# Kernel optimization log

Hardware: AMD Instinct MI355X
Metric: run time of the kernel (lower is better)

## Reference

```python
import jax, jax.numpy as jnp
import numpy as np

TW = 25          # time_window
H = 128          # hidden_features
NL = 6           # hidden_layer
N = 8192         # batch*n_nodes
E = 131072       # edges (avg degree 16)
EDGE_DIM = 51    # 50 (u diff) + 1 (pos_x diff)
LEM_IN = 4       # pos_x, u_ch0, u_ch1, ts
PDE_L = 16.0
PDE_TMAX = 4.0
PDE_DT = 0.04
NEG_SLOPE = 0.2  # PyG GATConv leaky_relu slope


def swish(x):
    return x * jax.nn.sigmoid(x)


def setup_inputs() -> dict:
    key = jax.random.key(0)
    ks = jax.random.split(key, 32)
    def p(k, shape, s=0.05):
        return jax.random.normal(k, shape, jnp.float32) * s
    inp = {}
    inp['u'] = jax.random.normal(ks[0], (N, 2 * TW), jnp.float32)
    inp['pos'] = jax.random.uniform(ks[1], (N, 2), jnp.float32)
    inp['edge_index'] = jax.random.randint(ks[2], (2, E), 0, N)
    # LEM cell params (inp2hid: 4H, hid2hid: 3H, transform_z: H)
    inp['lem_inp_w'] = p(ks[3], (4 * H, LEM_IN)); inp['lem_inp_b'] = jnp.zeros(4 * H, jnp.float32)
    inp['lem_hid_w'] = p(ks[4], (3 * H, H));      inp['lem_hid_b'] = jnp.zeros(3 * H, jnp.float32)
    inp['lem_z_w'] = p(ks[5], (H, H));            inp['lem_z_b'] = jnp.zeros(H, jnp.float32)
    # lemoutput_mlp
    inp['mlp1_w'] = p(ks[6], (H, H)); inp['mlp1_b'] = jnp.zeros(H, jnp.float32)
    inp['mlp2_w'] = p(ks[7], (H, H)); inp['mlp2_b'] = jnp.zeros(H, jnp.float32)
    # main GAT layers (stacked over NL)
    inp['gnn_lin_w'] = p(ks[8], (NL, H, H)); inp['gnn_edge_w'] = p(ks[9], (NL, H, EDGE_DIM))
    inp['gnn_att_src'] = p(ks[10], (NL, H)); inp['gnn_att_dst'] = p(ks[11], (NL, H))
    inp['gnn_att_edge'] = p(ks[12], (NL, H)); inp['gnn_bias'] = jnp.zeros((NL, H), jnp.float32)
    # gate GAT layers
    inp['gate_lin_w'] = p(ks[13], (NL, H, H)); inp['gate_edge_w'] = p(ks[14], (NL, H, EDGE_DIM))
    inp['gate_att_src'] = p(ks[15], (NL, H)); inp['gate_att_dst'] = p(ks[16], (NL, H))
    inp['gate_att_edge'] = p(ks[17], (NL, H)); inp['gate_bias'] = jnp.zeros((NL, H), jnp.float32)
    # double_mlp + conv1d decoder (time_window==25 branch)
    inp['dbl_w'] = p(ks[18], (2 * H, H)); inp['dbl_b'] = jnp.zeros(2 * H, jnp.float32)
    inp['conv1_w'] = p(ks[19], (8, 2, 16)); inp['conv1_b'] = jnp.zeros(8, jnp.float32)
    inp['conv2_w'] = p(ks[20], (2, 8, 14)); inp['conv2_b'] = jnp.zeros(2, jnp.float32)
    return inp


def _gat(x, src, dst, edge_attr, lin_w, edge_w, a_src, a_dst, a_edge, bias):
    """Single-head GATConv with edge features (PyG semantics, aggregate at dst)."""
    xt = x @ lin_w.T                      # [N,H]
    et = edge_attr @ edge_w.T             # [E,H]
    logits = jax.nn.leaky_relu((xt @ a_src)[src] + (xt @ a_dst)[dst] + et @ a_edge, NEG_SLOPE)
    amax = jax.ops.segment_max(logits, dst, num_segments=N)
    amax = jnp.where(jnp.isfinite(amax), amax, 0.0)
    ex = jnp.exp(logits - amax[dst])
    denom = jax.ops.segment_sum(ex, dst, num_segments=N)
    w = ex / (denom[dst] + 1e-16)         # edge softmax over incoming edges
    out = jax.ops.segment_sum(w[:, None] * xt[src], dst, num_segments=N)
    return out + bias


def _forward(u, pos, lem_inp_w, lem_inp_b, lem_hid_w, lem_hid_b, lem_z_w, lem_z_b,
             mlp1_w, mlp1_b, mlp2_w, mlp2_b,
             gnn_lin_w, gnn_edge_w, gnn_att_src, gnn_att_dst, gnn_att_edge, gnn_bias,
             gate_lin_w, gate_edge_w, gate_att_src, gate_att_dst, gate_att_edge, gate_bias,
             dbl_w, dbl_b, conv1_w, conv1_b, conv2_w, conv2_b, edge_index):
    pos_x = pos[:, 1:2] / PDE_L    # [N,1]
    pos_t = pos[:, 0:1] / PDE_TMAX # [N,1]
    dt = jnp.cumsum(jnp.full((TW,), PDE_DT, jnp.float32))  # [TW]
    ts = pos_t + dt[None, :]       # [N,TW]
    # LEM input: [TW, N, 4] = (pos_x, u channel 0, u channel 1, ts)
    lem_x = jnp.concatenate([
        jnp.broadcast_to(pos_x[None, :, :], (TW, N, 1)),
        u[:, :TW].T[:, :, None],
        u[:, TW:].T[:, :, None],
        ts.T[:, :, None],
    ], axis=-1)

    def cell(carry, xt):
        y, z = carry
        ii = xt @ lem_inp_w.T + lem_inp_b   # [N,4H]
        hh = y @ lem_hid_w.T + lem_hid_b    # [N,3H]
        i1, i2, i3, i4 = jnp.split(ii, 4, axis=-1)
        h1, h2, h3 = jnp.split(hh, 3, axis=-1)
        ms_dt_bar = jax.nn.sigmoid(i1 + h1)
        ms_dt = jax.nn.sigmoid(i2 + h2)
        z = (1.0 - ms_dt) * z + ms_dt * jnp.tanh(i3 + h3)
        y = (1.0 - ms_dt_bar) * y + ms_dt_bar * jnp.tanh(z @ lem_z_w.T + lem_z_b + i4)
        return (y, z), None

    y0 = jnp.zeros((N, H), u.dtype)
    (y, _), _ = jax.lax.scan(cell, (y0, y0), lem_x)
    h = swish(y @ mlp1_w.T + mlp1_b)
    h = swish(h @ mlp2_w.T + mlp2_b)

    src, dst = edge_index[0], edge_index[1]
    edge_attr = jnp.concatenate([u[src] - u[dst], pos_x[src] - pos_x[dst]], axis=-1)  # [E,51]

    for i in range(NL):
        tau = jax.nn.sigmoid(_gat(h, src, dst, edge_attr, gate_lin_w[i], gate_edge_w[i],
                                  gate_att_src[i], gate_att_dst[i], gate_att_edge[i], gate_bias[i]))
        msg = swish(_gat(h, src, dst, edge_attr, gnn_lin_w[i], gnn_edge_w[i],
                         gnn_att_src[i], gnn_att_dst[i], gnn_att_edge[i], gnn_bias[i]))
        h = (1.0 - tau) * h + tau * msg

    h2 = swish(h @ dbl_w.T + dbl_b).reshape(N, 2, H)  # [N,2,128]
    dn = ('NCH', 'OIH', 'NCH')
    d = jax.lax.conv_general_dilated(h2, conv1_w, (3,), 'VALID', dimension_numbers=dn)
    d = swish(d + conv1_b[None, :, None])              # [N,8,38]
    d = jax.lax.conv_general_dilated(d, conv2_w, (1,), 'VALID', dimension_numbers=dn)
    d = d + conv2_b[None, :, None]                     # [N,2,25]
    out = u.reshape(N, 2, TW) + dt[None, None, :] * d
    return out.reshape(N, 2 * TW)


def reference(u, pos, edge_index, lem_inp_w, lem_inp_b, lem_hid_w, lem_hid_b, lem_z_w, lem_z_b,
              mlp1_w, mlp1_b, mlp2_w, mlp2_b,
              gnn_lin_w, gnn_edge_w, gnn_att_src, gnn_att_dst, gnn_att_edge, gnn_bias,
              gate_lin_w, gate_edge_w, gate_att_src, gate_att_dst, gate_att_edge, gate_bias,
              dbl_w, dbl_b, conv1_w, conv1_b, conv2_w, conv2_b):
    return _forward(u, pos, lem_inp_w, lem_inp_b, lem_hid_w, lem_hid_b, lem_z_w, lem_z_b,
                    mlp1_w, mlp1_b, mlp2_w, mlp2_b,
                    gnn_lin_w, gnn_edge_w, gnn_att_src, gnn_att_dst, gnn_att_edge, gnn_bias,
                    gate_lin_w, gate_edge_w, gate_att_src, gate_att_dst, gate_att_edge, gate_bias,
                    dbl_w, dbl_b, conv1_w, conv1_b, conv2_w, conv2_b, edge_index)
```

## Files before the change

kernel.cpp:

```cpp
#include <hip/hip_runtime.h>

#define N_NODES 8192
#define N_EDGES 131072

using short8 = __attribute__((ext_vector_type(8))) short;
using f32x4  = __attribute__((ext_vector_type(4))) float;

__device__ __forceinline__ float rcpf(float x){ return __builtin_amdgcn_rcpf(x); }
__device__ __forceinline__ float sigm(float x){ return rcpf(1.0f+__expf(-x)); }
__device__ __forceinline__ float ftanh(float x){ float e=__expf(2.0f*x); return (e-1.0f)*rcpf(e+1.0f); }
__device__ __forceinline__ float swishf(float x){ return x*sigm(x); }
__device__ __forceinline__ float leaky(float x){ return x>=0.0f? x : 0.2f*x; }
__device__ __forceinline__ float dot4(float4 a, float4 b){ return a.x*b.x+a.y*b.y+a.z*b.z+a.w*b.w; }
__device__ __forceinline__ short f2bf(float x){
  unsigned u=__float_as_uint(x);
  unsigned r=(u + 0x7fffu + ((u>>16)&1u))>>16;
  return (short)r;
}
__device__ __forceinline__ int pack2bf(float a, float b){
  return (int)(((unsigned)(unsigned short)f2bf(a)) | (((unsigned)(unsigned short)f2bf(b))<<16));
}

__device__ __forceinline__ float wave_rmax(float v){
  #pragma unroll
  for(int m=32;m;m>>=1) v=fmaxf(v,__shfl_xor(v,m));
  return v;
}
__device__ __forceinline__ float wave_rsum(float v){
  #pragma unroll
  for(int m=32;m;m>>=1) v+=__shfl_xor(v,m);
  return v;
}

__global__ __launch_bounds__(256) void hist_kernel(const int* __restrict__ dst, int* __restrict__ cnt){
  int e=blockIdx.x*256+threadIdx.x;
  if(e<N_EDGES) atomicAdd(&cnt[dst[e]],1);
}

__global__ __launch_bounds__(1024) void scan_kernel(const int* __restrict__ cnt, int* __restrict__ rowptr, int* __restrict__ cursor){
  __shared__ int sums[1024];
  int t=threadIdx.x; int base=t*8;
  int local[8]; int s=0;
  #pragma unroll
  for(int i=0;i<8;++i){ local[i]=s; s+=cnt[base+i]; }
  sums[t]=s; __syncthreads();
  for(int off=1;off<1024;off<<=1){
    int v=(t>=off)?sums[t-off]:0;
    __syncthreads();
    sums[t]+=v;
    __syncthreads();
  }
  int offset=(t>0)?sums[t-1]:0;
  #pragma unroll
  for(int i=0;i<8;++i){ int v=offset+local[i]; rowptr[base+i]=v; cursor[base+i]=v; }
  if(t==1023) rowptr[N_NODES]=sums[1023];
}

__global__ __launch_bounds__(256) void scatter_kernel(const int* __restrict__ src, const int* __restrict__ dst,
                                                      int* __restrict__ cursor, int* __restrict__ csr_src){
  int e=blockIdx.x*256+threadIdx.x;
  if(e<N_EDGES){
    int slot=atomicAdd(&cursor[dst[e]],1);
    csr_src[slot]=src[e];
  }
}

__global__ __launch_bounds__(256) void prep_bf16_kernel(
    const float* __restrict__ lem_hid_w, const float* __restrict__ lem_z_w,
    const float* __restrict__ mlp1_w, const float* __restrict__ mlp2_w,
    const float* __restrict__ gate_lin_w, const float* __restrict__ gnn_lin_w,
    short* __restrict__ whb, short* __restrict__ wzb, short* __restrict__ w1b,
    short* __restrict__ w2b, short* __restrict__ wlin16)
{
  int i=blockIdx.x*256+threadIdx.x;
  if(i<49152){ whb[i]=f2bf(lem_hid_w[i]); return; }
  if(i<65536){ int k=i-49152; wzb[k]=f2bf(lem_z_w[k]); return; }
  if(i<81920){ int k=i-65536; w1b[k]=f2bf(mlp1_w[k]); return; }
  if(i<98304){ int k=i-81920; w2b[k]=f2bf(mlp2_w[k]); return; }
  int k=i-98304;
  int l=k>>15, which=(k>>14)&1, r=k&16383;
  const float* s = which? gnn_lin_w + l*16384 + r : gate_lin_w + l*16384 + r;
  wlin16[k]=f2bf(*s);
}

__global__ __launch_bounds__(256) void we_kernel(const float* __restrict__ gate_ew, const float* __restrict__ gnn_ew,
                                                 const float* __restrict__ gate_ae, const float* __restrict__ gnn_ae,
                                                 float* __restrict__ we){
  int idx=blockIdx.x*256+threadIdx.x;
  if(idx>=12*51) return;
  int g=idx/51, k=idx%51, l=g>>1;
  const float* ew = (g&1)? gnn_ew + l*128*51 : gate_ew + l*128*51;
  const float* ae = (g&1)? gnn_ae + l*128    : gate_ae + l*128;
  float s=0.f;
  for(int f=0;f<128;++f) s+=ew[f*51+k]*ae[f];
  we[idx]=s;
}

__global__ __launch_bounds__(128) void gsc_kernel(const float* __restrict__ u, const float* __restrict__ pos,
                                                  const float* __restrict__ we, float* __restrict__ gsc){
  int n=blockIdx.x*128+threadIdx.x;
  float uv[50];
  #pragma unroll
  for(int k=0;k<50;++k) uv[k]=u[n*50+k];
  float px=pos[n*2+1]*(1.0f/16.0f);
  for(int g=0;g<12;++g){
    const float* w=we+g*51;
    float s=w[50]*px;
    #pragma unroll
    for(int k=0;k<50;++k) s+=w[k]*uv[k];
    gsc[g*N_NODES+n]=s;
  }
}

__global__ __launch_bounds__(512,2) void lem_mfma2_kernel(
    const float* __restrict__ u, const float* __restrict__ pos,
    const float* __restrict__ Wi, const float* __restrict__ bi,
    const short* __restrict__ whb, const float* __restrict__ bh,
    const short* __restrict__ wzb, const float* __restrict__ bz,
    const short* __restrict__ w1b, const float* __restrict__ b1,
    const short* __restrict__ w2b, const float* __restrict__ b2,
    float* __restrict__ hout)
{
  __shared__ short y16[16*128];
  __shared__ short z16[16*128];
  __shared__ float u_s[16*50];
  __shared__ float hstg[16*132];

  const int tid=threadIdx.x, lane=tid&63, w=tid>>6;
  const int node=lane&15, q=lane>>4;
  const int n7=node&7;
  const int n0=blockIdx.x*16;

  for(int i=tid;i<16*50;i+=512) u_s[i]=u[n0*50+i];
  for(int i=tid;i<16*64;i+=512) ((int*)y16)[i]=0;

  const float px = pos[(n0+node)*2+1]*(1.0f/16.0f);
  const float pt = pos[(n0+node)*2+0]*0.25f;

  float cbase[4][4], cslope[4][4], ca[4][4], cb[4][4];
  #pragma unroll
  for(int gg=0; gg<4; ++gg){
    #pragma unroll
    for(int r=0;r<4;++r){
      int fr = w*16+q*4+r;
      int row = gg*128+fr;
      float4 wi = *(const float4*)(Wi+4*row);
      float bb = bi[row] + ((gg<3)? bh[row] : bz[fr]);
      cbase[gg][r] = bb + wi.x*px + wi.w*pt;
      cslope[gg][r]= wi.w*0.04f;
      ca[gg][r]=wi.y; cb[gg][r]=wi.z;
    }
  }

  short8 whf[3][4];
  #pragma unroll
  for(int gg=0;gg<3;++gg)
    #pragma unroll
    for(int kk=0;kk<4;++kk)
      whf[gg][kk]=*(const short8*)(whb + (gg*128 + w*16 + node)*128 + kk*32 + q*8);
  short8 wzf[4];
  #pragma unroll
  for(int kk=0;kk<4;++kk)
    wzf[kk]=*(const short8*)(wzb + (w*16 + node)*128 + kk*32 + q*8);

  float yreg[4]={0.f,0.f,0.f,0.f}, zreg[4]={0.f,0.f,0.f,0.f};
  float msb[4], i4s[4];
  const int wrslot = (w*16+q*4) ^ (n7<<3);
  __syncthreads();

  for(int t=0;t<25;++t){
    f32x4 h1a={0.f,0.f,0.f,0.f}, h2a=h1a, h3a=h1a;
    #pragma unroll
    for(int kk=0;kk<4;++kk){
      short8 yb=*(const short8*)&y16[node*128 + ((kk*32 + q*8) ^ (n7<<3))];
      h1a=__builtin_amdgcn_mfma_f32_16x16x32_bf16(whf[0][kk],yb,h1a,0,0,0);
      h2a=__builtin_amdgcn_mfma_f32_16x16x32_bf16(whf[1][kk],yb,h2a,0,0,0);
      h3a=__builtin_amdgcn_mfma_f32_16x16x32_bf16(whf[2][kk],yb,h3a,0,0,0);
    }
    const float u0=u_s[node*50+t], u1=u_s[node*50+25+t];
    const float tf=(float)(t+1);
    #pragma unroll
    for(int r=0;r<4;++r){
      float i1=cbase[0][r]+cslope[0][r]*tf+ca[0][r]*u0+cb[0][r]*u1;
      float i2=cbase[1][r]+cslope[1][r]*tf+ca[1][r]*u0+cb[1][r]*u1;
      float i3=cbase[2][r]+cslope[2][r]*tf+ca[2][r]*u0+cb[2][r]*u1;
      i4s[r]  =cbase[3][r]+cslope[3][r]*tf+ca[3][r]*u0+cb[3][r]*u1;
      msb[r]=sigm(i1+h1a[r]);
      float ms=sigm(i2+h2a[r]);
      zreg[r]=(1.0f-ms)*zreg[r]+ms*ftanh(i3+h3a[r]);
    }
    { int2 zz; zz.x=pack2bf(zreg[0],zreg[1]); zz.y=pack2bf(zreg[2],zreg[3]);
      *(int2*)&z16[node*128 + wrslot]=zz; }
    __syncthreads();
    f32x4 zw={0.f,0.f,0.f,0.f};
    #pragma unroll
    for(int kk=0;kk<4;++kk){
      short8 zb=*(const short8*)&z16[node*128 + ((kk*32 + q*8) ^ (n7<<3))];
      zw=__builtin_amdgcn_mfma_f32_16x16x32_bf16(wzf[kk],zb,zw,0,0,0);
    }
    #pragma unroll
    for(int r=0;r<4;++r)
      yreg[r]=(1.0f-msb[r])*yreg[r]+msb[r]*ftanh(zw[r]+i4s[r]);
    { int2 yy; yy.x=pack2bf(yreg[0],yreg[1]); yy.y=pack2bf(yreg[2],yreg[3]);
      *(int2*)&y16[node*128 + wrslot]=yy; }
    __syncthreads();
  }

  {
    short8 w1f[4];
    #pragma unroll
    for(int kk=0;kk<4;++kk)
      w1f[kk]=*(const short8*)(w1b + (w*16 + node)*128 + kk*32 + q*8);
    float4 b1v=*(const float4*)(b1 + w*16 + q*4);
    f32x4 a={0.f,0.f,0.f,0.f};
    #pragma unroll
    for(int kk=0;kk<4;++kk){
      short8 yb=*(const short8*)&y16[node*128 + ((kk*32 + q*8) ^ (n7<<3))];
      a=__builtin_amdgcn_mfma_f32_16x16x32_bf16(w1f[kk],yb,a,0,0,0);
    }
    float t0=swishf(a[0]+b1v.x), t1=swishf(a[1]+b1v.y);
    float t2=swishf(a[2]+b1v.z), t3=swishf(a[3]+b1v.w);
    int2 zz; zz.x=pack2bf(t0,t1); zz.y=pack2bf(t2,t3);
    *(int2*)&z16[node*128 + wrslot]=zz;
  }
  __syncthreads();
  {
    short8 w2f[4];
    #pragma unroll
    for(int kk=0;kk<4;++kk)
      w2f[kk]=*(const short8*)(w2b + (w*16 + node)*128 + kk*32 + q*8);
    float4 b2v=*(const float4*)(b2 + w*16 + q*4);
    f32x4 a={0.f,0.f,0.f,0.f};
    #pragma unroll
    for(int kk=0;kk<4;++kk){
      short8 zb=*(const short8*)&z16[node*128 + ((kk*32 + q*8) ^ (n7<<3))];
      a=__builtin_amdgcn_mfma_f32_16x16x32_bf16(w2f[kk],zb,a,0,0,0);
    }
    hstg[node*132 + w*16+q*4+0]=swishf(a[0]+b2v.x);
    hstg[node*132 + w*16+q*4+1]=swishf(a[1]+b2v.y);
    hstg[node*132 + w*16+q*4+2]=swishf(a[2]+b2v.z);
    hstg[node*132 + w*16+q*4+3]=swishf(a[3]+b2v.w);
  }
  __syncthreads();
  for(int i=tid;i<16*128;i+=512){
    int nn=i>>7, ff=i&127;
    hout[(n0+nn)*128+ff]=hstg[nn*132+ff];
  }
}

__global__ __launch_bounds__(256) void gat_transform_mfma(
    const float* __restrict__ h,
    const short* __restrict__ wl,
    const float* __restrict__ a_sg, const float* __restrict__ a_dg,
    const float* __restrict__ a_sm, const float* __restrict__ a_dm,
    const float* __restrict__ gsc_g, const float* __restrict__ gsc_m,
    short* __restrict__ xt16, float* __restrict__ ss2, float* __restrict__ sd2)
{
  __shared__ short h16[32*128];
  __shared__ short xts[32*256];
  const int tid=threadIdx.x, lane=tid&63, w=tid>>6;
  const int rt=w&1, cg=w>>1;
  const int r16=lane&15, kq=lane>>4;
  const int n0=blockIdx.x*32;

  {
    const float4* hp=(const float4*)(h + (size_t)n0*128) + tid*4;
    int row=tid>>3, e0=(tid&7)*16;
    #pragma unroll
    for(int c=0;c<2;++c){
      float4 v0=hp[2*c], v1=hp[2*c+1];
      short8 s;
      s[0]=f2bf(v0.x); s[1]=f2bf(v0.y); s[2]=f2bf(v0.z); s[3]=f2bf(v0.w);
      s[4]=f2bf(v1.x); s[5]=f2bf(v1.y); s[6]=f2bf(v1.z); s[7]=f2bf(v1.w);
      *(short8*)&h16[row*128 + ((e0+8*c) ^ ((row&7)<<3))]=s;
    }
  }
  __syncthreads();
  short8 afr[4];
  {
    int row=rt*16+r16;
    #pragma unroll
    for(int kk=0;kk<4;++kk)
      afr[kk]=*(const short8*)&h16[row*128 + ((kk*32+kq*8) ^ ((row&7)<<3))];
  }
  const short* wb = wl + cg*16384;
  const float* as_ = cg? a_sm : a_sg;
  const float* ad_ = cg? a_dm : a_dg;
  float ssp[4]={0,0,0,0}, sdp[4]={0,0,0,0};
  #pragma unroll
  for(int ct=0;ct<8;++ct){
    int c0=ct*16;
    f32x4 acc={0.f,0.f,0.f,0.f};
    #pragma unroll
    for(int kk=0;kk<4;++kk){
      short8 b=*(const short8*)(wb + (c0+r16)*128 + kk*32 + kq*8);
      acc=__builtin_amdgcn_mfma_f32_16x16x32_bf16(afr[kk],b,acc,0,0,0);
    }
    float av=as_[c0+r16], dv=ad_[c0+r16];
    #pragma unroll
    for(int r=0;r<4;++r){
      ssp[r]+=acc[r]*av; sdp[r]+=acc[r]*dv;
      xts[(rt*16+kq*4+r)*256 + cg*128 + c0 + r16]=f2bf(acc[r]);
    }
  }
  #pragma unroll
  for(int m=1;m<16;m<<=1){
    #pragma unroll
    for(int r=0;r<4;++r){
      ssp[r]+=__shfl_xor(ssp[r],m);
      sdp[r]+=__shfl_xor(sdp[r],m);
    }
  }
  if(r16==0){
    #pragma unroll
    for(int r=0;r<4;++r){
      int n=n0+rt*16+kq*4+r;
      float gv = (cg? gsc_m : gsc_g)[n];
      ss2[2*n+cg]=ssp[r]+gv;
      sd2[2*n+cg]=sdp[r]-gv;
    }
  }
  __syncthreads();
  const short8* sp=(const short8*)xts;
  short8* dp=(short8*)(xt16 + (size_t)n0*256);
  for(int i=tid;i<32*256/8;i+=256) dp[i]=sp[i];
}

__global__ __launch_bounds__(256) void gat_aggregate2(
    const int* __restrict__ rowptr, const int* __restrict__ csr_src,
    const short* __restrict__ xt16,
    const float* __restrict__ ss2, const float* __restrict__ sd2,
    const float* __restrict__ bias_g, const float* __restrict__ bias_m,
    float* __restrict__ h)
{
  __shared__ float4 stg[4][64];
  const int lane=threadIdx.x&63, w=threadIdx.x>>6;
  const int n=blockIdx.x*4+w;
  const int s0=rowptr[n], deg=rowptr[n+1]-s0;
  const float2 sdv=*(const float2*)(sd2+2*n);
  const float bg=sdv.x, bm=sdv.y;

  float mg=-1e30f, mm=-1e30f;
  int sc=0; float lgc=0.f, lmc=0.f;
  for(int c=0;c<deg;c+=64){
    int i=c+lane;
    if(i<deg){
      int s=csr_src[s0+i];
      float2 ssv=*(const float2*)(ss2+2*s);
      float lg=leaky(ssv.x+bg), lm=leaky(ssv.y+bm);
      if(c==0){sc=s; lgc=lg; lmc=lm;}
      mg=fmaxf(mg,lg); mm=fmaxf(mm,lm);
    }
  }
  mg=wave_rmax(mg); mm=wave_rmax(mm);

  float dg=0.f, dm=0.f;
  float acc0=0.f,acc1=0.f,acc2=0.f,acc3=0.f;
  for(int c=0;c<deg;c+=64){
    int i=c+lane;
    int s=sc; float lg=lgc, lm=lmc;
    if(c>0 && i<deg){
      s=csr_src[s0+i];
      float2 ssv=*(const float2*)(ss2+2*s);
      lg=leaky(ssv.x+bg); lm=leaky(ssv.y+bm);
    }
    float eg=0.f, em=0.f;
    if(i<deg){ eg=__expf(lg-mg); em=__expf(lm-mm); dg+=eg; dm+=em; }
    float4 st; st.x=__int_as_float(s); st.y=eg; st.z=em; st.w=0.f;
    stg[w][lane]=st;
    __threadfence_block();
    int cntc=min(64,deg-c);
    for(int j=0;j<cntc;++j){
      float4 e=stg[w][j];
      int sj=__float_as_int(e.x);
      float wgt = lane<32 ? e.y : e.z;
      const unsigned* xp=(const unsigned*)(xt16 + (size_t)sj*256 + 4*lane);
      unsigned p0=xp[0], p1=xp[1];
      acc0 += wgt*__uint_as_float(p0<<16);
      acc1 += wgt*__uint_as_float(p0&0xffff0000u);
      acc2 += wgt*__uint_as_float(p1<<16);
      acc3 += wgt*__uint_as_float(p1&0xffff0000u);
    }
  }
  dg=wave_rsum(dg); dm=wave_rsum(dm);
  float rr = lane<32? rcpf(dg+1e-16f) : rcpf(dm+1e-16f);
  const float* bp = lane<32 ? bias_g + 4*lane : bias_m + 4*(lane-32);
  float4 bv=*(const float4*)bp;
  float o0=acc0*rr+bv.x, o1=acc1*rr+bv.y, o2=acc2*rr+bv.z, o3=acc3*rr+bv.w;
  float s0_=sigm(o0), s1_=sigm(o1), s2_=sigm(o2), s3_=sigm(o3);
  float v0 = lane<32? s0_ : o0*s0_;
  float v1 = lane<32? s1_ : o1*s1_;
  float v2 = lane<32? s2_ : o2*s2_;
  float v3 = lane<32? s3_ : o3*s3_;
  float m0=__shfl_xor(v0,32), m1=__shfl_xor(v1,32), m2=__shfl_xor(v2,32), m3=__shfl_xor(v3,32);
  if(lane<32){
    float4 hv=*(const float4*)(h + (size_t)n*128 + 4*lane);
    hv.x=(1.0f-v0)*hv.x+v0*m0;
    hv.y=(1.0f-v1)*hv.y+v1*m1;
    hv.z=(1.0f-v2)*hv.z+v2*m2;
    hv.w=(1.0f-v3)*hv.w+v3*m3;
    *(float4*)(h + (size_t)n*128 + 4*lane)=hv;
  }
}

__global__ __launch_bounds__(256) void decoder_kernel(
    const float* __restrict__ h, const float* __restrict__ u,
    const float* __restrict__ Wd, const float* __restrict__ bd,
    const float* __restrict__ w1, const float* __restrict__ b1,
    const float* __restrict__ w2, const float* __restrict__ b2,
    float* __restrict__ out)
{
  __shared__ float h_lds[8][128];
  __shared__ float h2[8][2][128];
  __shared__ float c1[8][8][38];
  __shared__ float w1s[256], w2s[224], b1s[8], b2s[2];
  const int tid=threadIdx.x;
  const int n0=blockIdx.x*8;
  for(int i=tid;i<8*128;i+=256) ((float*)h_lds)[i]=h[n0*128+i];
  w1s[tid]=w1[tid];
  if(tid<224) w2s[tid]=w2[tid];
  if(tid<8) b1s[tid]=b1[tid];
  if(tid<2) b2s[tid]=b2[tid];
  __syncthreads();
  {
    const float4* wp=(const float4*)(Wd + tid*128);
    float acc[8];
    #pragma unroll
    for(int n=0;n<8;++n)acc[n]=0.f;
    for(int k=0;k<32;++k){
      float4 w=wp[k];
      #pragma unroll
      for(int n=0;n<8;++n){ float4 hv=*(const float4*)&h_lds[n][k*4]; acc[n]+=dot4(w,hv); }
    }
    float bdv=bd[tid];
    int ch=tid>>7, p=tid&127;
    #pragma unroll
    for(int n=0;n<8;++n) h2[n][ch][p]=swishf(acc[n]+bdv);
  }
  __syncthreads();
  for(int idx=tid; idx<8*8*38; idx+=256){
    int n=idx/(8*38); int r=idx%(8*38); int oc=r/38, p=r%38;
    float acc=b1s[oc];
    const float* ww=&w1s[oc*32];
    #pragma unroll
    for(int ic=0;ic<2;++ic)
      #pragma unroll
      for(int k=0;k<16;++k) acc+=ww[ic*16+k]*h2[n][ic][3*p+k];
    c1[n][oc][p]=swishf(acc);
  }
  __syncthreads();
  for(int idx=tid; idx<8*2*25; idx+=256){
    int n=idx/50; int r=idx%50; int oc=r/25, p=r%25;
    float acc=b2s[oc];
    const float* ww=&w2s[oc*112];
    #pragma unroll
    for(int ic=0;ic<8;++ic)
      #pragma unroll
      for(int k=0;k<14;++k) acc+=ww[ic*14+k]*c1[n][ic][p+k];
    int col=oc*25+p;
    out[(n0+n)*50+col]=u[(n0+n)*50+col]+0.04f*(float)(p+1)*acc;
  }
}

extern "C" void kernel_launch(void* const* d_in, const int* in_sizes, int n_in,
                              void* d_out, int out_size, void* d_ws, size_t ws_size,
                              hipStream_t stream)
{
  const float* u          =(const float*)d_in[0];
  const float* pos        =(const float*)d_in[1];
  const int*   ei         =(const int*)d_in[2];
  const float* lem_inp_w  =(const float*)d_in[3];
  const float* lem_inp_b  =(const float*)d_in[4];
  const float* lem_hid_w  =(const float*)d_in[5];
  const float* lem_hid_b  =(const float*)d_in[6];
  const float* lem_z_w    =(const float*)d_in[7];
  const float* lem_z_b    =(const float*)d_in[8];
  const float* mlp1_w     =(const float*)d_in[9];
  const float* mlp1_b     =(const float*)d_in[10];
  const float* mlp2_w     =(const float*)d_in[11];
  const float* mlp2_b     =(const float*)d_in[12];
  const float* gnn_lin_w  =(const float*)d_in[13];
  const float* gnn_edge_w =(const float*)d_in[14];
  const float* gnn_att_src=(const float*)d_in[15];
  const float* gnn_att_dst=(const float*)d_in[16];
  const float* gnn_att_edge=(const float*)d_in[17];
  const float* gnn_bias   =(const float*)d_in[18];
  const float* gate_lin_w =(const float*)d_in[19];
  const float* gate_edge_w=(const float*)d_in[20];
  const float* gate_att_src=(const float*)d_in[21];
  const float* gate_att_dst=(const float*)d_in[22];
  const float* gate_att_edge=(const float*)d_in[23];
  const float* gate_bias  =(const float*)d_in[24];
  const float* dbl_w      =(const float*)d_in[25];
  const float* dbl_b      =(const float*)d_in[26];
  const float* conv1_w    =(const float*)d_in[27];
  const float* conv1_b    =(const float*)d_in[28];
  const float* conv2_w    =(const float*)d_in[29];
  const float* conv2_b    =(const float*)d_in[30];
  float* out=(float*)d_out;

  char* ws=(char*)d_ws;
  size_t off=0;
  auto alloc=[&](size_t bytes)->char*{ char* p=ws+off; off+=(bytes+255)&~(size_t)255; return p; };
  float* h    =(float*)alloc((size_t)N_NODES*128*4);
  short* xt16 =(short*)alloc((size_t)N_NODES*256*2);
  float* ss2  =(float*)alloc((size_t)N_NODES*2*4);
  float* sd2  =(float*)alloc((size_t)N_NODES*2*4);
  float* gsc  =(float*)alloc((size_t)12*N_NODES*4);
  float* wearr=(float*)alloc(12*51*4);
  int* cnt    =(int*)alloc(N_NODES*4);
  int* rowptr =(int*)alloc((N_NODES+8)*4);
  int* cursor =(int*)alloc(N_NODES*4);
  int* csrsrc =(int*)alloc((size_t)N_EDGES*4);
  short* whb  =(short*)alloc(384*128*2);
  short* wzb  =(short*)alloc(128*128*2);
  short* w1b  =(short*)alloc(128*128*2);
  short* w2b  =(short*)alloc(128*128*2);
  short* wlin16=(short*)alloc((size_t)6*2*128*128*2);

  const int* src=ei;
  const int* dst=ei+N_EDGES;

  hipMemsetAsync(cnt,0,N_NODES*4,stream);
  hist_kernel<<<N_EDGES/256,256,0,stream>>>(dst,cnt);
  scan_kernel<<<1,1024,0,stream>>>(cnt,rowptr,cursor);
  scatter_kernel<<<N_EDGES/256,256,0,stream>>>(src,dst,cursor,csrsrc);
  prep_bf16_kernel<<<(294912+255)/256,256,0,stream>>>(lem_hid_w,lem_z_w,mlp1_w,mlp2_w,
                                                      gate_lin_w,gnn_lin_w,
                                                      whb,wzb,w1b,w2b,wlin16);
  we_kernel<<<3,256,0,stream>>>(gate_edge_w,gnn_edge_w,gate_att_edge,gnn_att_edge,wearr);
  gsc_kernel<<<N_NODES/128,128,0,stream>>>(u,pos,wearr,gsc);
  lem_mfma2_kernel<<<N_NODES/16,512,0,stream>>>(u,pos,lem_inp_w,lem_inp_b,whb,lem_hid_b,
                                                wzb,lem_z_b,w1b,mlp1_b,w2b,mlp2_b,h);
  for(int l=0;l<6;++l){
    gat_transform_mfma<<<N_NODES/32,256,0,stream>>>(h,
      wlin16+(size_t)l*2*16384,
      gate_att_src+l*128, gate_att_dst+l*128,
      gnn_att_src+l*128, gnn_att_dst+l*128,
      gsc+(size_t)(2*l)*N_NODES, gsc+(size_t)(2*l+1)*N_NODES,
      xt16, ss2, sd2);
    gat_aggregate2<<<N_NODES/4,256,0,stream>>>(rowptr,csrsrc,xt16,ss2,sd2,
      gate_bias+l*128, gnn_bias+l*128, h);
  }
  decoder_kernel<<<N_NODES/8,256,0,stream>>>(h,u,dbl_w,dbl_b,conv1_w,conv1_b,conv2_w,conv2_b,out);
}
```

Before: 424.0 us.

## Fuse GAT aggregate with next layer transform and last layer with decoder

Each GAT layer's aggregation is merged with the following layer's linear transform in one kernel, using double-buffered xt/ss/sd arrays. The LEM kernel now also runs the first transform, and the last aggregation is merged with the decoder. This cuts the kernel count from 14 to 7 and removes the fp32 h reload and bf16 conversion between stages. The aggregation also switches from an LDS staging loop to shuffles with batched 8-row gathers. The trade-off is heavier 512-thread blocks that each handle only 16 nodes, which may reduce occupancy and MFMA efficiency in the transform.

```diff
diff --git a/kernel.cpp b/kernel.cpp
--- a/kernel.cpp
+++ b/kernel.cpp
@@ -112,19 +112,168 @@
   }
 }
 
-__global__ __launch_bounds__(512,2) void lem_mfma2_kernel(
+__device__ __forceinline__ void transform_phase(
+    int tid, int n0,
+    const short* __restrict__ h16, short* __restrict__ xts,
+    float* __restrict__ ssred, float* __restrict__ sdred,
+    const short* __restrict__ wl,
+    const float* __restrict__ a_sg, const float* __restrict__ a_dg,
+    const float* __restrict__ a_sm, const float* __restrict__ a_dm,
+    const float* __restrict__ gsc_g, const float* __restrict__ gsc_m,
+    short* __restrict__ xt_out, float* __restrict__ ss_out, float* __restrict__ sd_out)
+{
+  const int lane=tid&63, w=tid>>6;
+  const int cg=w&1, ch=w>>1;
+  const int r16=lane&15, kq=lane>>4;
+  __syncthreads();
+  short8 afr[4];
+  #pragma unroll
+  for(int kk=0;kk<4;++kk)
+    afr[kk]=*(const short8*)&h16[r16*128 + ((kk*32+kq*8) ^ ((r16&7)<<3))];
+  const short* wb = wl + cg*16384;
+  const float* as_ = cg? a_sm : a_sg;
+  const float* ad_ = cg? a_dm : a_dg;
+  float ssp[4]={0,0,0,0}, sdp[4]={0,0,0,0};
+  #pragma unroll
+  for(int ci=0;ci<2;++ci){
+    int c0=(ch*2+ci)*16;
+    f32x4 acc={0.f,0.f,0.f,0.f};
+    #pragma unroll
+    for(int kk=0;kk<4;++kk){
+      short8 b=*(const short8*)(wb + (c0+r16)*128 + kk*32 + kq*8);
+      acc=__builtin_amdgcn_mfma_f32_16x16x32_bf16(afr[kk],b,acc,0,0,0);
+    }
+    float av=as_[c0+r16], dv=ad_[c0+r16];
+    #pragma unroll
+    for(int r=0;r<4;++r){
+      ssp[r]+=acc[r]*av; sdp[r]+=acc[r]*dv;
+      xts[(kq*4+r)*256 + cg*128 + c0 + r16]=f2bf(acc[r]);
+    }
+  }
+  #pragma unroll
+  for(int m=1;m<16;m<<=1){
+    #pragma unroll
+    for(int r=0;r<4;++r){ ssp[r]+=__shfl_xor(ssp[r],m); sdp[r]+=__shfl_xor(sdp[r],m); }
+  }
+  if(r16==0){
+    #pragma unroll
+    for(int r=0;r<4;++r){ ssred[w*16+kq*4+r]=ssp[r]; sdred[w*16+kq*4+r]=sdp[r]; }
+  }
+  __syncthreads();
+  if(tid<32){
+    int node=tid&15, cg2=tid>>4;
+    float sv=0.f, dv=0.f;
+    #pragma unroll
+    for(int c2=0;c2<4;++c2){ sv+=ssred[(c2*2+cg2)*16+node]; dv+=sdred[(c2*2+cg2)*16+node]; }
+    float gv=(cg2? gsc_m:gsc_g)[n0+node];
+    ss_out[2*(n0+node)+cg2]=sv+gv;
+    sd_out[2*(n0+node)+cg2]=dv-gv;
+  }
+  {
+    const short8* sp=(const short8*)xts;
+    short8* dp=(short8*)(xt_out + (size_t)n0*256);
+    dp[tid]=sp[tid];
+  }
+}
+
+__device__ __forceinline__ float4 aggregate_node(
+    int n, int lane,
+    const int* __restrict__ rowptr, const int* __restrict__ csr_src,
+    const short* __restrict__ xt_in, const float* __restrict__ ss_in, const float* __restrict__ sd_in,
+    const float* __restrict__ bias_g, const float* __restrict__ bias_m,
+    const float* __restrict__ h)
+{
+  const int s0=rowptr[n], deg=rowptr[n+1]-s0;
+  const float2 sdv=*(const float2*)(sd_in+2*n);
+  const float bg=sdv.x, bm=sdv.y;
+  float mg=-1e30f, mm=-1e30f;
+  for(int c=0;c<deg;c+=64){
+    int i=c+lane;
+    if(i<deg){
+      int s=csr_src[s0+i];
+      float2 ssv=*(const float2*)(ss_in+2*s);
+      mg=fmaxf(mg,leaky(ssv.x+bg)); mm=fmaxf(mm,leaky(ssv.y+bm));
+    }
+  }
+  mg=wave_rmax(mg); mm=wave_rmax(mm);
+  float dg=0.f,dm=0.f, acc0=0.f,acc1=0.f,acc2=0.f,acc3=0.f;
+  for(int c=0;c<deg;c+=64){
+    int i=c+lane, s=0; float eg=0.f, em=0.f;
+    if(i<deg){
+      s=csr_src[s0+i];
+      float2 ssv=*(const float2*)(ss_in+2*s);
+      eg=__expf(leaky(ssv.x+bg)-mg); em=__expf(leaky(ssv.y+bm)-mm);
+      dg+=eg; dm+=em;
+    }
+    int cntc=min(64,deg-c);
+    for(int cb=0;cb<cntc;cb+=8){
+      int sj[8]; float wj[8];
+      #pragma unroll
+      for(int jj=0;jj<8;++jj){
+        int idx=cb+jj;
+        int sv=__shfl(s,idx);
+        float wg=__shfl(eg,idx), wm=__shfl(em,idx);
+        sj[jj]=sv;
+        wj[jj]= lane<32? wg : wm;
+      }
+      uint2 rows[8];
+      #pragma unroll
+      for(int jj=0;jj<8;++jj)
+        rows[jj]=*(const uint2*)(xt_in + (size_t)sj[jj]*256 + 4*lane);
+      #pragma unroll
+      for(int jj=0;jj<8;++jj){
+        float wv=wj[jj];
+        unsigned p0=rows[jj].x, p1=rows[jj].y;
+        acc0+=wv*__uint_as_float(p0<<16);
+        acc1+=wv*__uint_as_float(p0&0xffff0000u);
+        acc2+=wv*__uint_as_float(p1<<16);
+        acc3+=wv*__uint_as_float(p1&0xffff0000u);
+      }
+    }
+  }
+  dg=wave_rsum(dg); dm=wave_rsum(dm);
+  float rr = lane<32? rcpf(dg+1e-16f) : rcpf(dm+1e-16f);
+  const float* bp = lane<32? bias_g+4*lane : bias_m+4*(lane-32);
+  float4 bv=*(const float4*)bp;
+  float o0=acc0*rr+bv.x, o1=acc1*rr+bv.y, o2=acc2*rr+bv.z, o3=acc3*rr+bv.w;
+  float s0_=sigm(o0), s1_=sigm(o1), s2_=sigm(o2), s3_=sigm(o3);
+  float v0=lane<32? s0_:o0*s0_;
+  float v1=lane<32? s1_:o1*s1_;
+  float v2=lane<32? s2_:o2*s2_;
+  float v3=lane<32? s3_:o3*s3_;
+  float m0=__shfl_xor(v0,32), m1=__shfl_xor(v1,32), m2=__shfl_xor(v2,32), m3=__shfl_xor(v3,32);
+  float4 r;
+  if(lane<32){
+    float4 hv=*(const float4*)(h + (size_t)n*128 + 4*lane);
+    r.x=(1.0f-v0)*hv.x+v0*m0;
+    r.y=(1.0f-v1)*hv.y+v1*m1;
+    r.z=(1.0f-v2)*hv.z+v2*m2;
+    r.w=(1.0f-v3)*hv.w+v3*m3;
+  } else { r.x=r.y=r.z=r.w=0.f; }
+  return r;
+}
+
+__global__ __launch_bounds__(512,2) void lem_t0_kernel(
     const float* __restrict__ u, const float* __restrict__ pos,
     const float* __restrict__ Wi, const float* __restrict__ bi,
     const short* __restrict__ whb, const float* __restrict__ bh,
     const short* __restrict__ wzb, const float* __restrict__ bz,
     const short* __restrict__ w1b, const float* __restrict__ b1,
     const short* __restrict__ w2b, const float* __restrict__ b2,
-    float* __restrict__ hout)
+    float* __restrict__ hout,
+    const short* __restrict__ wl,
+    const float* __restrict__ a_sg, const float* __restrict__ a_dg,
+    const float* __restrict__ a_sm, const float* __restrict__ a_dm,
+    const float* __restrict__ gsc_g, const float* __restrict__ gsc_m,
+    short* __restrict__ xt_out, float* __restrict__ ss_out, float* __restrict__ sd_out)
 {
   __shared__ short y16[16*128];
   __shared__ short z16[16*128];
   __shared__ float u_s[16*50];
   __shared__ float hstg[16*132];
+  __shared__ short h16[16*128];
+  __shared__ short xts[16*256];
+  __shared__ float ssred[128], sdred[128];
 
   const int tid=threadIdx.x, lane=tid&63, w=tid>>6;
   const int node=lane&15, q=lane>>4;
@@ -236,209 +385,97 @@
       short8 zb=*(const short8*)&z16[node*128 + ((kk*32 + q*8) ^ (n7<<3))];
       a=__builtin_amdgcn_mfma_f32_16x16x32_bf16(w2f[kk],zb,a,0,0,0);
     }
-    hstg[node*132 + w*16+q*4+0]=swishf(a[0]+b2v.x);
-    hstg[node*132 + w*16+q*4+1]=swishf(a[1]+b2v.y);
-    hstg[node*132 + w*16+q*4+2]=swishf(a[2]+b2v.z);
-    hstg[node*132 + w*16+q*4+3]=swishf(a[3]+b2v.w);
+    float h0=swishf(a[0]+b2v.x), h1=swishf(a[1]+b2v.y);
+    float h2=swishf(a[2]+b2v.z), h3=swishf(a[3]+b2v.w);
+    hstg[node*132 + w*16+q*4+0]=h0;
+    hstg[node*132 + w*16+q*4+1]=h1;
+    hstg[node*132 + w*16+q*4+2]=h2;
+    hstg[node*132 + w*16+q*4+3]=h3;
+    int2 hb; hb.x=pack2bf(h0,h1); hb.y=pack2bf(h2,h3);
+    *(int2*)&h16[node*128 + wrslot]=hb;
   }
   __syncthreads();
   for(int i=tid;i<16*128;i+=512){
     int nn=i>>7, ff=i&127;
     hout[(n0+nn)*128+ff]=hstg[nn*132+ff];
   }
-}
-
-__global__ __launch_bounds__(256) void gat_transform_mfma(
-    const float* __restrict__ h,
+  transform_phase(tid,n0,h16,xts,ssred,sdred,wl,a_sg,a_dg,a_sm,a_dm,gsc_g,gsc_m,xt_out,ss_out,sd_out);
+}
+
+__global__ __launch_bounds__(512,2) void gat_fused_kernel(
+    const int* __restrict__ rowptr, const int* __restrict__ csr_src,
+    const short* __restrict__ xt_in, const float* __restrict__ ss_in, const float* __restrict__ sd_in,
+    const float* __restrict__ bias_g, const float* __restrict__ bias_m,
+    float* __restrict__ h,
     const short* __restrict__ wl,
     const float* __restrict__ a_sg, const float* __restrict__ a_dg,
     const float* __restrict__ a_sm, const float* __restrict__ a_dm,
     const float* __restrict__ gsc_g, const float* __restrict__ gsc_m,
-    short* __restrict__ xt16, float* __restrict__ ss2, float* __restrict__ sd2)
+    short* __restrict__ xt_out, float* __restrict__ ss_out, float* __restrict__ sd_out)
 {
-  __shared__ short h16[32*128];
-  __shared__ short xts[32*256];
+  __shared__ short h16[16*128];
+  __shared__ short xts[16*256];
+  __shared__ float ssred[128], sdred[128];
   const int tid=threadIdx.x, lane=tid&63, w=tid>>6;
-  const int rt=w&1, cg=w>>1;
-  const int r16=lane&15, kq=lane>>4;
-  const int n0=blockIdx.x*32;
-
-  {
-    const float4* hp=(const float4*)(h + (size_t)n0*128) + tid*4;
-    int row=tid>>3, e0=(tid&7)*16;
-    #pragma unroll
-    for(int c=0;c<2;++c){
-      float4 v0=hp[2*c], v1=hp[2*c+1];
-      short8 s;
-      s[0]=f2bf(v0.x); s[1]=f2bf(v0.y); s[2]=f2bf(v0.z); s[3]=f2bf(v0.w);
-      s[4]=f2bf(v1.x); s[5]=f2bf(v1.y); s[6]=f2bf(v1.z); s[7]=f2bf(v1.w);
-      *(short8*)&h16[row*128 + ((e0+8*c) ^ ((row&7)<<3))]=s;
-    }
-  }
-  __syncthreads();
-  short8 afr[4];
-  {
-    int row=rt*16+r16;
-    #pragma unroll
-    for(int kk=0;kk<4;++kk)
-      afr[kk]=*(const short8*)&h16[row*128 + ((kk*32+kq*8) ^ ((row&7)<<3))];
-  }
-  const short* wb = wl + cg*16384;
-  const float* as_ = cg? a_sm : a_sg;
-  const float* ad_ = cg? a_dm : a_dg;
-  float ssp[4]={0,0,0,0}, sdp[4]={0,0,0,0};
-  #pragma unroll
-  for(int ct=0;ct<8;++ct){
-    int c0=ct*16;
-    f32x4 acc={0.f,0.f,0.f,0.f};
-    #pragma unroll
-    for(int kk=0;kk<4;++kk){
-      short8 b=*(const short8*)(wb + (c0+r16)*128 + kk*32 + kq*8);
-      acc=__builtin_amdgcn_mfma_f32_16x16x32_bf16(afr[kk],b,acc,0,0,0);
-    }
-    float av=as_[c0+r16], dv=ad_[c0+r16];
-    #pragma unroll
-    for(int r=0;r<4;++r){
-      ssp[r]+=acc[r]*av; sdp[r]+=acc[r]*dv;
-      xts[(rt*16+kq*4+r)*256 + cg*128 + c0 + r16]=f2bf(acc[r]);
-    }
-  }
-  #pragma unroll
-  for(int m=1;m<16;m<<=1){
-    #pragma unroll
-    for(int r=0;r<4;++r){
-      ssp[r]+=__shfl_xor(ssp[r],m);
-      sdp[r]+=__shfl_xor(sdp[r],m);
-    }
-  }
-  if(r16==0){
-    #pragma unroll
-    for(int r=0;r<4;++r){
-      int n=n0+rt*16+kq*4+r;
-      float gv = (cg? gsc_m : gsc_g)[n];
-      ss2[2*n+cg]=ssp[r]+gv;
-      sd2[2*n+cg]=sdp[r]-gv;
-    }
-  }
-  __syncthreads();
-  const short8* sp=(const short8*)xts;
-  short8* dp=(short8*)(xt16 + (size_t)n0*256);
-  for(int i=tid;i<32*256/8;i+=256) dp[i]=sp[i];
-}
-
-__global__ __launch_bounds__(256) void gat_aggregate2(
+  const int n0=blockIdx.x*16;
+  #pragma unroll
+  for(int which=0;which<2;++which){
+    int row=w*2+which, n=n0+row;
+    float4 hv=aggregate_node(n,lane,rowptr,csr_src,xt_in,ss_in,sd_in,bias_g,bias_m,h);
+    if(lane<32){
+      *(float4*)(h+(size_t)n*128+4*lane)=hv;
+      int2 hb; hb.x=pack2bf(hv.x,hv.y); hb.y=pack2bf(hv.z,hv.w);
+      *(int2*)&h16[row*128 + ((4*lane) ^ ((row&7)<<3))]=hb;
+    }
+  }
+  transform_phase(tid,n0,h16,xts,ssred,sdred,wl,a_sg,a_dg,a_sm,a_dm,gsc_g,gsc_m,xt_out,ss_out,sd_out);
+}
+
+__global__ __launch_bounds__(512,2) void gat_last_decoder_kernel(
     const int* __restrict__ rowptr, const int* __restrict__ csr_src,
-    const short* __restrict__ xt16,
-    const float* __restrict__ ss2, const float* __restrict__ sd2,
+    const short* __restrict__ xt_in, const float* __restrict__ ss_in, const float* __restrict__ sd_in,
     const float* __restrict__ bias_g, const float* __restrict__ bias_m,
-    float* __restrict__ h)
-{
-  __shared__ float4 stg[4][64];
-  const int lane=threadIdx.x&63, w=threadIdx.x>>6;
-  const int n=blockIdx.x*4+w;
-  const int s0=rowptr[n], deg=rowptr[n+1]-s0;
-  const float2 sdv=*(const float2*)(sd2+2*n);
-  const float bg=sdv.x, bm=sdv.y;
-
-  float mg=-1e30f, mm=-1e30f;
-  int sc=0; float lgc=0.f, lmc=0.f;
-  for(int c=0;c<deg;c+=64){
-    int i=c+lane;
-    if(i<deg){
-      int s=csr_src[s0+i];
-      float2 ssv=*(const float2*)(ss2+2*s);
-      float lg=leaky(ssv.x+bg), lm=leaky(ssv.y+bm);
-      if(c==0){sc=s; lgc=lg; lmc=lm;}
-      mg=fmaxf(mg,lg); mm=fmaxf(mm,lm);
-    }
-  }
-  mg=wave_rmax(mg); mm=wave_rmax(mm);
-
-  float dg=0.f, dm=0.f;
-  float acc0=0.f,acc1=0.f,acc2=0.f,acc3=0.f;
-  for(int c=0;c<deg;c+=64){
-    int i=c+lane;
-    int s=sc; float lg=lgc, lm=lmc;
-    if(c>0 && i<deg){
-      s=csr_src[s0+i];
-      float2 ssv=*(const float2*)(ss2+2*s);
-      lg=leaky(ssv.x+bg); lm=leaky(ssv.y+bm);
-    }
-    float eg=0.f, em=0.f;
-    if(i<deg){ eg=__expf(lg-mg); em=__expf(lm-mm); dg+=eg; dm+=em; }
-    float4 st; st.x=__int_as_float(s); st.y=eg; st.z=em; st.w=0.f;
-    stg[w][lane]=st;
-    __threadfence_block();
-    int cntc=min(64,deg-c);
-    for(int j=0;j<cntc;++j){
-      float4 e=stg[w][j];
-      int sj=__float_as_int(e.x);
-      float wgt = lane<32 ? e.y : e.z;
-      const unsigned* xp=(const unsigned*)(xt16 + (size_t)sj*256 + 4*lane);
-      unsigned p0=xp[0], p1=xp[1];
-      acc0 += wgt*__uint_as_float(p0<<16);
-      acc1 += wgt*__uint_as_float(p0&0xffff0000u);
-      acc2 += wgt*__uint_as_float(p1<<16);
-      acc3 += wgt*__uint_as_float(p1&0xffff0000u);
-    }
-  }
-  dg=wave_rsum(dg); dm=wave_rsum(dm);
-  float rr = lane<32? rcpf(dg+1e-16f) : rcpf(dm+1e-16f);
-  const float* bp = lane<32 ? bias_g + 4*lane : bias_m + 4*(lane-32);
-  float4 bv=*(const float4*)bp;
-  float o0=acc0*rr+bv.x, o1=acc1*rr+bv.y, o2=acc2*rr+bv.z, o3=acc3*rr+bv.w;
-  float s0_=sigm(o0), s1_=sigm(o1), s2_=sigm(o2), s3_=sigm(o3);
-  float v0 = lane<32? s0_ : o0*s0_;
-  float v1 = lane<32? s1_ : o1*s1_;
-  float v2 = lane<32? s2_ : o2*s2_;
-  float v3 = lane<32? s3_ : o3*s3_;
-  float m0=__shfl_xor(v0,32), m1=__shfl_xor(v1,32), m2=__shfl_xor(v2,32), m3=__shfl_xor(v3,32);
-  if(lane<32){
-    float4 hv=*(const float4*)(h + (size_t)n*128 + 4*lane);
-    hv.x=(1.0f-v0)*hv.x+v0*m0;
-    hv.y=(1.0f-v1)*hv.y+v1*m1;
-    hv.z=(1.0f-v2)*hv.z+v2*m2;
-    hv.w=(1.0f-v3)*hv.w+v3*m3;
-    *(float4*)(h + (size_t)n*128 + 4*lane)=hv;
-  }
-}
-
-__global__ __launch_bounds__(256) void decoder_kernel(
     const float* __restrict__ h, const float* __restrict__ u,
     const float* __restrict__ Wd, const float* __restrict__ bd,
     const float* __restrict__ w1, const float* __restrict__ b1,
     const float* __restrict__ w2, const float* __restrict__ b2,
     float* __restrict__ out)
 {
-  __shared__ float h_lds[8][128];
-  __shared__ float h2[8][2][128];
-  __shared__ float c1[8][8][38];
+  __shared__ float hdec[16*128];
+  __shared__ float h2[16][2][128];
+  __shared__ float c1[16][8][38];
   __shared__ float w1s[256], w2s[224], b1s[8], b2s[2];
-  const int tid=threadIdx.x;
-  const int n0=blockIdx.x*8;
-  for(int i=tid;i<8*128;i+=256) ((float*)h_lds)[i]=h[n0*128+i];
-  w1s[tid]=w1[tid];
-  if(tid<224) w2s[tid]=w2[tid];
-  if(tid<8) b1s[tid]=b1[tid];
-  if(tid<2) b2s[tid]=b2[tid];
+  const int tid=threadIdx.x, lane=tid&63, w=tid>>6;
+  const int n0=blockIdx.x*16;
+  if(tid<256) w1s[tid]=w1[tid];
+  else if(tid<480) w2s[tid-256]=w2[tid-256];
+  else if(tid<488) b1s[tid-480]=b1[tid-480];
+  else if(tid<490) b2s[tid-488]=b2[tid-488];
+  #pragma unroll
+  for(int which=0;which<2;++which){
+    int row=w*2+which, n=n0+row;
+    float4 hv=aggregate_node(n,lane,rowptr,csr_src,xt_in,ss_in,sd_in,bias_g,bias_m,h);
+    if(lane<32) *(float4*)&hdec[row*128+4*lane]=hv;
+  }
   __syncthreads();
   {
-    const float4* wp=(const float4*)(Wd + tid*128);
+    int o=tid&255, grp=tid>>8;
+    const float4* wp=(const float4*)(Wd + o*128);
     float acc[8];
     #pragma unroll
-    for(int n=0;n<8;++n)acc[n]=0.f;
+    for(int n=0;n<8;++n) acc[n]=0.f;
     for(int k=0;k<32;++k){
-      float4 w=wp[k];
+      float4 wv=wp[k];
       #pragma unroll
-      for(int n=0;n<8;++n){ float4 hv=*(const float4*)&h_lds[n][k*4]; acc[n]+=dot4(w,hv); }
-    }
-    float bdv=bd[tid];
-    int ch=tid>>7, p=tid&127;
-    #pragma unroll
-    for(int n=0;n<8;++n) h2[n][ch][p]=swishf(acc[n]+bdv);
-  }
-  __syncthreads();
-  for(int idx=tid; idx<8*8*38; idx+=256){
+      for(int n=0;n<8;++n){ float4 hval=*(const float4*)&hdec[(grp*8+n)*128+k*4]; acc[n]+=dot4(wv,hval); }
+    }
+    float bdv=bd[o];
+    int chn=o>>7, p=o&127;
+    #pragma unroll
+    for(int n=0;n<8;++n) h2[grp*8+n][chn][p]=swishf(acc[n]+bdv);
+  }
+  __syncthreads();
+  for(int idx=tid; idx<16*8*38; idx+=512){
     int n=idx/(8*38); int r=idx%(8*38); int oc=r/38, p=r%38;
     float acc=b1s[oc];
     const float* ww=&w1s[oc*32];
@@ -449,7 +486,7 @@
     c1[n][oc][p]=swishf(acc);
   }
   __syncthreads();
-  for(int idx=tid; idx<8*2*25; idx+=256){
+  for(int idx=tid; idx<16*2*25; idx+=512){
     int n=idx/50; int r=idx%50; int oc=r/25, p=r%25;
     float acc=b2s[oc];
     const float* ww=&w2s[oc*112];
@@ -503,9 +540,12 @@
   size_t off=0;
   auto alloc=[&](size_t bytes)->char*{ char* p=ws+off; off+=(bytes+255)&~(size_t)255; return p; };
   float* h    =(float*)alloc((size_t)N_NODES*128*4);
-  short* xt16 =(short*)alloc((size_t)N_NODES*256*2);
-  float* ss2  =(float*)alloc((size_t)N_NODES*2*4);
-  float* sd2  =(float*)alloc((size_t)N_NODES*2*4);
+  short* xtA  =(short*)alloc((size_t)N_NODES*256*2);
+  short* xtB  =(short*)alloc((size_t)N_NODES*256*2);
+  float* ssA  =(float*)alloc((size_t)N_NODES*2*4);
+  float* ssB  =(float*)alloc((size_t)N_NODES*2*4);
+  float* sdA  =(float*)alloc((size_t)N_NODES*2*4);
+  float* sdB  =(float*)alloc((size_t)N_NODES*2*4);
   float* gsc  =(float*)alloc((size_t)12*N_NODES*4);
   float* wearr=(float*)alloc(12*51*4);
   int* cnt    =(int*)alloc(N_NODES*4);
@@ -530,17 +570,32 @@
                                                       whb,wzb,w1b,w2b,wlin16);
   we_kernel<<<3,256,0,stream>>>(gate_edge_w,gnn_edge_w,gate_att_edge,gnn_att_edge,wearr);
   gsc_kernel<<<N_NODES/128,128,0,stream>>>(u,pos,wearr,gsc);
-  lem_mfma2_kernel<<<N_NODES/16,512,0,stream>>>(u,pos,lem_inp_w,lem_inp_b,whb,lem_hid_b,
-                                                wzb,lem_z_b,w1b,mlp1_b,w2b,mlp2_b,h);
-  for(int l=0;l<6;++l){
-    gat_transform_mfma<<<N_NODES/32,256,0,stream>>>(h,
-      wlin16+(size_t)l*2*16384,
-      gate_att_src+l*128, gate_att_dst+l*128,
-      gnn_att_src+l*128, gnn_att_dst+l*128,
-      gsc+(size_t)(2*l)*N_NODES, gsc+(size_t)(2*l+1)*N_NODES,
-      xt16, ss2, sd2);
-    gat_aggregate2<<<N_NODES/4,256,0,stream>>>(rowptr,csrsrc,xt16,ss2,sd2,
-      gate_bias+l*128, gnn_bias+l*128, h);
-  }
-  decoder_kernel<<<N_NODES/8,256,0,stream>>>(h,u,dbl_w,dbl_b,conv1_w,conv1_b,conv2_w,conv2_b,out);
-}
+
+  short* xtbuf[2]={xtA,xtB};
+  float* ssbuf[2]={ssA,ssB};
+  float* sdbuf[2]={sdA,sdB};
+
+  lem_t0_kernel<<<N_NODES/16,512,0,stream>>>(u,pos,lem_inp_w,lem_inp_b,whb,lem_hid_b,
+      wzb,lem_z_b,w1b,mlp1_b,w2b,mlp2_b,h,
+      wlin16,
+      gate_att_src, gate_att_dst, gnn_att_src, gnn_att_dst,
+      gsc, gsc+(size_t)N_NODES,
+      xtbuf[0], ssbuf[0], sdbuf[0]);
+
+  for(int l=0;l<5;++l){
+    int in=l&1, o2=(l+1)&1;
+    gat_fused_kernel<<<N_NODES/16,512,0,stream>>>(rowptr,csrsrc,
+      xtbuf[in],ssbuf[in],sdbuf[in],
+      gate_bias+l*128, gnn_bias+l*128, h,
+      wlin16+(size_t)(l+1)*2*16384,
+      gate_att_src+(l+1)*128, gate_att_dst+(l+1)*128,
+      gnn_att_src+(l+1)*128, gnn_att_dst+(l+1)*128,
+      gsc+(size_t)(2*(l+1))*N_NODES, gsc+(size_t)(2*(l+1)+1)*N_NODES,
+      xtbuf[o2], ssbuf[o2], sdbuf[o2]);
+  }
+
+  gat_last_decoder_kernel<<<N_NODES/16,512,0,stream>>>(rowptr,csrsrc,
+      xtbuf[1],ssbuf[1],sdbuf[1],
+      gate_bias+5*128, gnn_bias+5*128, h, u,
+      dbl_w, dbl_b, conv1_w, conv1_b, conv2_w, conv2_b, out);
+}
```

After: 376.1 us. -11.3%, faster.
